# Kernel tuning notes

Measured on AMD Instinct MI355X. Metric: run time of the kernel, lower is better.

## Reference

```python
import jax, jax.numpy as jnp
import numpy as np


def setup_inputs() -> dict:
    key = jax.random.key(0)
    ks = jax.random.split(key, 5)
    B, T, I, H, O = 64, 1024, 128, 256, 128
    stdv = 1.0 / np.sqrt(H)
    return {
        "x": jax.random.normal(ks[0], (B, T, I), dtype=jnp.float32),
        "W": jax.random.uniform(ks[1], (I, 4 * H), dtype=jnp.float32, minval=-stdv, maxval=stdv),
        "U": jax.random.uniform(ks[2], (H, 4 * H), dtype=jnp.float32, minval=-stdv, maxval=stdv),
        "bias": jax.random.uniform(ks[3], (4 * H,), dtype=jnp.float32, minval=-stdv, maxval=stdv),
        "dense_w": jax.random.uniform(ks[4], (O, H), dtype=jnp.float32, minval=-stdv, maxval=stdv),
        "dense_b": jnp.zeros((O,), dtype=jnp.float32),
    }


def reference(x, W, U, bias, dense_w, dense_b):
    B, T, I = x.shape
    H = U.shape[0]
    # Precompute input contribution for all timesteps in one big GEMM.
    xW = jnp.einsum("bti,ig->btg", x, W) + bias  # (B, T, 4H)

    def step(carry, xw_t):
        h, c = carry
        gates = xw_t + h @ U  # (B, 4H)
        i_t = jax.nn.sigmoid(gates[:, :H])
        f_t = jax.nn.sigmoid(gates[:, H:2 * H])
        g_t = jnp.tanh(gates[:, 2 * H:3 * H])
        o_t = jax.nn.sigmoid(gates[:, 3 * H:])
        c = f_t * c + i_t * g_t
        h = o_t * jnp.tanh(c)
        return (h, c), h

    h0 = jnp.zeros((B, H), dtype=x.dtype)
    c0 = jnp.zeros((B, H), dtype=x.dtype)
    (h_T, _), _ = jax.lax.scan(step, (h0, c0), jnp.swapaxes(xW, 0, 1))
    # Original takes hidden_seq[:, -1, :] == final h_t, then Linear, then unsqueeze(2).
    out = h_T @ dense_w.T + dense_b  # (B, O)
    return out[:, :, None]  # (B, O, 1)
```

## Files before the change

### kernel.cpp

```cpp
#include <hip/hip_runtime.h>
#include <math.h>

#define TT 1024
#define BB 64
#define II 128
#define HH 256
#define OO 128
#define GPB 16
#define NCOL 64
#define Z_STRIDE 392
#define PART_BG_STRIDE 68
#define PART_RC_STRIDE 273

#define WS_HBUF_B 16384
#define WS_CLEAR_B (WS_HBUF_B + 2 * BB * HH * 8)

typedef unsigned long long u64;
typedef unsigned int u32;

__device__ __forceinline__ float rcp(float v) { return __builtin_amdgcn_rcpf(v); }
__device__ __forceinline__ float sigm(float v) { return rcp(1.f + __expf(-v)); }
__device__ __forceinline__ float ftanh(float v) {
    return __builtin_fmaf(-2.f, rcp(__expf(2.f * v) + 1.f), 1.f);
}

extern "C" __global__ void __launch_bounds__(256, 1) lstm_scan(
    const float* __restrict__ x, const float* __restrict__ W,
    const float* __restrict__ U, const float* __restrict__ bias,
    float* __restrict__ wsf)
{
    __shared__ float z[4 * Z_STRIDE];
    __shared__ float part[16 * PART_RC_STRIDE];
    __shared__ int   misc[8];

    int* abortp = (int*)wsf;
    u64* hbuf   = (u64*)((char*)wsf + WS_HBUF_B);

    const int tid  = threadIdx.x;
    const int gid  = blockIdx.x & 15;
    const int p    = blockIdx.x >> 4;
    const int cg   = tid & 15;
    const int rc   = tid >> 4;
    const int lane = tid & 63;
    const int w    = tid >> 6;
    const int myb  = 4 * gid + w;
    const int j    = lane & 15;

    float wr[6][4][4];
    {
        const int c0 = cg * 4;
        const int gcol = (c0 >> 4) * HH + p * 16 + (c0 & 15);
#pragma unroll
        for (int rr = 0; rr < 6; ++rr) {
#pragma unroll
            for (int i = 0; i < 4; ++i) {
                const int r = rr * 64 + rc * 4 + i;
                const float4 wv = (rr < 2)
                    ? *(const float4*)(W + (size_t)r * 1024 + gcol)
                    : *(const float4*)(U + (size_t)(r - II) * 1024 + gcol);
                wr[rr][i][0] = wv.x; wr[rr][i][1] = wv.y;
                wr[rr][i][2] = wv.z; wr[rr][i][3] = wv.w;
            }
        }
    }
    const float bia_reg = bias[(lane >> 4) * HH + p * 16 + j];
    float creg = 0.f;

    for (int idx = tid; idx < 4 * Z_STRIDE; idx += 256) z[idx] = 0.f;
    if (tid < 8) misc[tid] = 0;

    if (tid < 128) {
        const int b2 = tid >> 5, l2 = tid & 31;
        const float4 xv = *(const float4*)(
            x + ((size_t)(4 * gid + b2) * TT + 0) * II + 4 * l2);
        *(float4*)(z + b2 * Z_STRIDE + 4 * l2) = xv;
    }
    __syncthreads();

    for (int t = 1; t <= TT; ++t) {
        float acc[4][4];
#pragma unroll
        for (int a = 0; a < 4; ++a)
#pragma unroll
            for (int b = 0; b < 4; ++b) acc[a][b] = 0.f;

#pragma unroll
        for (int rr = 0; rr < 2; ++rr) {
#pragma unroll
            for (int bg = 0; bg < 4; ++bg) {
                const float4 zv = *(const float4*)(z + bg * Z_STRIDE + rr * 64 + rc * 4);
#pragma unroll
                for (int c = 0; c < 4; ++c)
                    acc[bg][c] += zv.x * wr[rr][0][c] + zv.y * wr[rr][1][c]
                                + zv.z * wr[rr][2][c] + zv.w * wr[rr][3][c];
            }
        }

        if (t > 1) {
            const u32 want = (u32)(t - 1);
            const u64* hsrc = hbuf + ((size_t)((t - 1) & 1) * BB + myb) * HH;
            u64 n0, n1, n2, n3;
            int it = 0, ab = 0;
            for (;;) {
                n0 = __hip_atomic_load(hsrc + lane,       __ATOMIC_RELAXED, __HIP_MEMORY_SCOPE_AGENT);
                n1 = __hip_atomic_load(hsrc + lane + 64,  __ATOMIC_RELAXED, __HIP_MEMORY_SCOPE_AGENT);
                n2 = __hip_atomic_load(hsrc + lane + 128, __ATOMIC_RELAXED, __HIP_MEMORY_SCOPE_AGENT);
                n3 = __hip_atomic_load(hsrc + lane + 192, __ATOMIC_RELAXED, __HIP_MEMORY_SCOPE_AGENT);
                const bool ok = ((u32)(n0 >> 32) == want) && ((u32)(n1 >> 32) == want)
                             && ((u32)(n2 >> 32) == want) && ((u32)(n3 >> 32) == want);
                if (__ballot(ok) == ~0ULL) break;
                if ((++it & 63) == 0) {
                    int abv = __hip_atomic_load(abortp, __ATOMIC_RELAXED,
                                                __HIP_MEMORY_SCOPE_AGENT);
                    if (abv) { ab = 1; break; }
                    if (it > (1 << 19)) {
                        if (lane == 0)
                            __hip_atomic_store(abortp, 1, __ATOMIC_RELAXED,
                                               __HIP_MEMORY_SCOPE_AGENT);
                        ab = 1; break;
                    }
                }
            }
            if (ab && lane == 0) misc[w] = 1;
            float* zdst = z + w * Z_STRIDE + II + lane;
            zdst[0]   = __uint_as_float((u32)n0);
            zdst[64]  = __uint_as_float((u32)n1);
            zdst[128] = __uint_as_float((u32)n2);
            zdst[192] = __uint_as_float((u32)n3);
        }
        __syncthreads();
        if (misc[0] | misc[1] | misc[2] | misc[3]) break;

#pragma unroll
        for (int rr = 2; rr < 6; ++rr) {
#pragma unroll
            for (int bg = 0; bg < 4; ++bg) {
                const float4 zv = *(const float4*)(z + bg * Z_STRIDE + rr * 64 + rc * 4);
#pragma unroll
                for (int c = 0; c < 4; ++c)
                    acc[bg][c] += zv.x * wr[rr][0][c] + zv.y * wr[rr][1][c]
                                + zv.z * wr[rr][2][c] + zv.w * wr[rr][3][c];
            }
        }

#pragma unroll
        for (int bg = 0; bg < 4; ++bg)
#pragma unroll
            for (int c = 0; c < 4; ++c)
                part[rc * PART_RC_STRIDE + bg * PART_BG_STRIDE + cg * 4 + c] = acc[bg][c];
        __syncthreads();

        float s = bia_reg;
#pragma unroll
        for (int r2 = 0; r2 < 16; ++r2)
            s += part[r2 * PART_RC_STRIDE + w * PART_BG_STRIDE + lane];

        const float sf = __shfl(s, j + 16);
        const float sg = __shfl(s, j + 32);
        const float so = __shfl(s, j + 48);
        if (lane < 16) {
            const float iv = sigm(s);
            const float fv = sigm(sf);
            const float gv = ftanh(sg);
            const float ov = sigm(so);
            creg = fv * creg + iv * gv;
            const float hv = ov * ftanh(creg);
            const u64 pk = ((u64)(u32)t << 32) | (u64)__float_as_uint(hv);
            __hip_atomic_store(
                hbuf + ((size_t)(t & 1) * BB + myb) * HH + p * 16 + j,
                pk, __ATOMIC_RELAXED, __HIP_MEMORY_SCOPE_AGENT);
        } else if (lane < 48 && t < TT) {
            const int l2 = lane - 16;
            const float4 xv = *(const float4*)(
                x + ((size_t)myb * TT + t) * II + 4 * l2);
            *(float4*)(z + w * Z_STRIDE + 4 * l2) = xv;
        }
        __syncthreads();
    }
}

extern "C" __global__ void __launch_bounds__(256) lstm_out(
    const float* __restrict__ wsf, const float* __restrict__ dw,
    const float* __restrict__ db, float* __restrict__ out)
{
    __shared__ float hs[256];
    __shared__ float red[256];
    const int b = blockIdx.x;
    const int tid = threadIdx.x;
    const u64* h0 = (const u64*)((const char*)wsf + WS_HBUF_B);
    hs[tid] = __uint_as_float((u32)h0[(size_t)b * HH + tid]);
    __syncthreads();
    const int o = tid & 127, half = tid >> 7;
    const float* wrow = dw + o * HH + half * 128;
    const float* hrow = hs + half * 128;
    float s = 0.f;
#pragma unroll
    for (int k = 0; k < 128; k += 4) {
        const float4 wv = *(const float4*)(wrow + k);
        s += hrow[k] * wv.x + hrow[k + 1] * wv.y + hrow[k + 2] * wv.z + hrow[k + 3] * wv.w;
    }
    red[tid] = s;
    __syncthreads();
    if (tid < 128)
        out[(size_t)b * OO + tid] = red[tid] + red[128 + tid] + db[tid];
}

extern "C" void kernel_launch(void* const* d_in, const int* in_sizes, int n_in,
                              void* d_out, int out_size, void* d_ws, size_t ws_size,
                              hipStream_t stream)
{
    const float* x    = (const float*)d_in[0];
    const float* W    = (const float*)d_in[1];
    const float* U    = (const float*)d_in[2];
    const float* bias = (const float*)d_in[3];
    const float* dw   = (const float*)d_in[4];
    const float* db   = (const float*)d_in[5];
    float* out = (float*)d_out;
    float* ws  = (float*)d_ws;

    hipMemsetAsync(d_ws, 0, WS_CLEAR_B, stream);
    hipLaunchKernelGGL(lstm_scan, dim3(256), dim3(256), 0, stream,
                       x, W, U, bias, ws);
    hipLaunchKernelGGL(lstm_out, dim3(64), dim3(256), 0, stream, ws, dw, db, out);
}
```

Baseline: 2.113 ms.

## Precompute x@W+bias with a separate GEMM kernel before the recurrent scan

Splits the input projection out of the persistent LSTM scan into a tiled GEMM kernel that writes x@W+bias to a 256MB workspace. The scan then only multiplies h by U each step and reads one precomputed gate value per thread, which shortens the per-step critical path and frees registers. The spin-wait also double-buffers its polling loads. The cost is an extra pass that writes and reads a large buffer through HBM. The old fused kernel is kept as a fallback when the workspace is too small.

```diff
diff --git a/kernel.cpp b/kernel.cpp
--- a/kernel.cpp
+++ b/kernel.cpp
@@ -9,11 +9,14 @@
 #define GPB 16
 #define NCOL 64
 #define Z_STRIDE 392
+#define ZS2 264
 #define PART_BG_STRIDE 68
 #define PART_RC_STRIDE 273
 
 #define WS_HBUF_B 16384
 #define WS_CLEAR_B (WS_HBUF_B + 2 * BB * HH * 8)
+#define WS_XW_B   524288
+#define WS_NEED   (524288ull + 268435456ull)
 
 typedef unsigned long long u64;
 typedef unsigned int u32;
@@ -23,13 +26,64 @@
 __device__ __forceinline__ float ftanh(float v) {
     return __builtin_fmaf(-2.f, rcp(__expf(2.f * v) + 1.f), 1.f);
 }
+#define HLOAD(p) __hip_atomic_load((p), __ATOMIC_RELAXED, __HIP_MEMORY_SCOPE_AGENT)
+
+extern "C" __global__ void __launch_bounds__(256) xw_gemm(
+    const float* __restrict__ x, const float* __restrict__ W,
+    const float* __restrict__ bias, float* __restrict__ xw)
+{
+    __shared__ float xs[64][65];
+    __shared__ float wt[64][68];
+    const int tid = threadIdx.x;
+    const int tx = tid & 15, ty = tid >> 4;
+    const int bm = blockIdx.x, bn = blockIdx.y;
+
+    float acc[4][4];
+#pragma unroll
+    for (int i = 0; i < 4; ++i)
+#pragma unroll
+        for (int jj = 0; jj < 4; ++jj) acc[i][jj] = 0.f;
+
+    for (int k0 = 0; k0 < 128; k0 += 64) {
+#pragma unroll
+        for (int l = 0; l < 4; ++l) {
+            const int e = tid + l * 256;
+            const int row = e >> 4, c4 = (e & 15) * 4;
+            *(float4*)&xs[row][c4] =
+                *(const float4*)(x + (size_t)(bm * 64 + row) * 128 + k0 + c4);
+            *(float4*)&wt[row][c4] =
+                *(const float4*)(W + (size_t)(k0 + row) * 1024 + bn * 64 + c4);
+        }
+        __syncthreads();
+#pragma unroll 16
+        for (int kk = 0; kk < 64; ++kk) {
+            const float4 bv = *(const float4*)&wt[kk][tx * 4];
+#pragma unroll
+            for (int i = 0; i < 4; ++i) {
+                const float av = xs[ty * 4 + i][kk];
+                acc[i][0] += av * bv.x; acc[i][1] += av * bv.y;
+                acc[i][2] += av * bv.z; acc[i][3] += av * bv.w;
+            }
+        }
+        __syncthreads();
+    }
+#pragma unroll
+    for (int i = 0; i < 4; ++i) {
+        const int row = bm * 64 + ty * 4 + i, col = bn * 64 + tx * 4;
+        float4 o;
+        o.x = acc[i][0] + bias[col];
+        o.y = acc[i][1] + bias[col + 1];
+        o.z = acc[i][2] + bias[col + 2];
+        o.w = acc[i][3] + bias[col + 3];
+        *(float4*)(xw + (size_t)row * 1024 + col) = o;
+    }
+}
 
 extern "C" __global__ void __launch_bounds__(256, 1) lstm_scan(
-    const float* __restrict__ x, const float* __restrict__ W,
-    const float* __restrict__ U, const float* __restrict__ bias,
+    const float* __restrict__ xw, const float* __restrict__ U,
     float* __restrict__ wsf)
 {
-    __shared__ float z[4 * Z_STRIDE];
+    __shared__ float z[4 * ZS2];
     __shared__ float part[16 * PART_RC_STRIDE];
     __shared__ int   misc[8];
 
@@ -46,72 +100,50 @@
     const int myb  = 4 * gid + w;
     const int j    = lane & 15;
 
-    float wr[6][4][4];
+    float wh[4][4][4];
     {
         const int c0 = cg * 4;
         const int gcol = (c0 >> 4) * HH + p * 16 + (c0 & 15);
 #pragma unroll
-        for (int rr = 0; rr < 6; ++rr) {
+        for (int rrh = 0; rrh < 4; ++rrh)
 #pragma unroll
             for (int i = 0; i < 4; ++i) {
-                const int r = rr * 64 + rc * 4 + i;
-                const float4 wv = (rr < 2)
-                    ? *(const float4*)(W + (size_t)r * 1024 + gcol)
-                    : *(const float4*)(U + (size_t)(r - II) * 1024 + gcol);
-                wr[rr][i][0] = wv.x; wr[rr][i][1] = wv.y;
-                wr[rr][i][2] = wv.z; wr[rr][i][3] = wv.w;
-            }
-        }
-    }
-    const float bia_reg = bias[(lane >> 4) * HH + p * 16 + j];
+                const int r = rrh * 64 + rc * 4 + i;
+                const float4 wv = *(const float4*)(U + (size_t)r * 1024 + gcol);
+                wh[rrh][i][0] = wv.x; wh[rrh][i][1] = wv.y;
+                wh[rrh][i][2] = wv.z; wh[rrh][i][3] = wv.w;
+            }
+    }
+    const int redcol = (lane >> 4) * HH + p * 16 + j;
     float creg = 0.f;
 
-    for (int idx = tid; idx < 4 * Z_STRIDE; idx += 256) z[idx] = 0.f;
+    for (int idx = tid; idx < 4 * ZS2; idx += 256) z[idx] = 0.f;
     if (tid < 8) misc[tid] = 0;
-
-    if (tid < 128) {
-        const int b2 = tid >> 5, l2 = tid & 31;
-        const float4 xv = *(const float4*)(
-            x + ((size_t)(4 * gid + b2) * TT + 0) * II + 4 * l2);
-        *(float4*)(z + b2 * Z_STRIDE + 4 * l2) = xv;
-    }
     __syncthreads();
 
+    float xwreg = xw[((size_t)myb * TT + 0) * 1024 + redcol];
+
     for (int t = 1; t <= TT; ++t) {
-        float acc[4][4];
-#pragma unroll
-        for (int a = 0; a < 4; ++a)
-#pragma unroll
-            for (int b = 0; b < 4; ++b) acc[a][b] = 0.f;
-
-#pragma unroll
-        for (int rr = 0; rr < 2; ++rr) {
-#pragma unroll
-            for (int bg = 0; bg < 4; ++bg) {
-                const float4 zv = *(const float4*)(z + bg * Z_STRIDE + rr * 64 + rc * 4);
-#pragma unroll
-                for (int c = 0; c < 4; ++c)
-                    acc[bg][c] += zv.x * wr[rr][0][c] + zv.y * wr[rr][1][c]
-                                + zv.z * wr[rr][2][c] + zv.w * wr[rr][3][c];
-            }
-        }
-
         if (t > 1) {
             const u32 want = (u32)(t - 1);
             const u64* hsrc = hbuf + ((size_t)((t - 1) & 1) * BB + myb) * HH;
             u64 n0, n1, n2, n3;
+            u64 a0 = HLOAD(hsrc + lane),       a1 = HLOAD(hsrc + lane + 64),
+                a2 = HLOAD(hsrc + lane + 128), a3 = HLOAD(hsrc + lane + 192);
             int it = 0, ab = 0;
             for (;;) {
-                n0 = __hip_atomic_load(hsrc + lane,       __ATOMIC_RELAXED, __HIP_MEMORY_SCOPE_AGENT);
-                n1 = __hip_atomic_load(hsrc + lane + 64,  __ATOMIC_RELAXED, __HIP_MEMORY_SCOPE_AGENT);
-                n2 = __hip_atomic_load(hsrc + lane + 128, __ATOMIC_RELAXED, __HIP_MEMORY_SCOPE_AGENT);
-                n3 = __hip_atomic_load(hsrc + lane + 192, __ATOMIC_RELAXED, __HIP_MEMORY_SCOPE_AGENT);
-                const bool ok = ((u32)(n0 >> 32) == want) && ((u32)(n1 >> 32) == want)
-                             && ((u32)(n2 >> 32) == want) && ((u32)(n3 >> 32) == want);
-                if (__ballot(ok) == ~0ULL) break;
+                u64 b0 = HLOAD(hsrc + lane),       b1 = HLOAD(hsrc + lane + 64),
+                    b2 = HLOAD(hsrc + lane + 128), b3 = HLOAD(hsrc + lane + 192);
+                bool ok = ((u32)(a0 >> 32) == want) && ((u32)(a1 >> 32) == want)
+                       && ((u32)(a2 >> 32) == want) && ((u32)(a3 >> 32) == want);
+                if (__ballot(ok) == ~0ULL) { n0 = a0; n1 = a1; n2 = a2; n3 = a3; break; }
+                a0 = HLOAD(hsrc + lane);       a1 = HLOAD(hsrc + lane + 64);
+                a2 = HLOAD(hsrc + lane + 128); a3 = HLOAD(hsrc + lane + 192);
+                ok = ((u32)(b0 >> 32) == want) && ((u32)(b1 >> 32) == want)
+                  && ((u32)(b2 >> 32) == want) && ((u32)(b3 >> 32) == want);
+                if (__ballot(ok) == ~0ULL) { n0 = b0; n1 = b1; n2 = b2; n3 = b3; break; }
                 if ((++it & 63) == 0) {
-                    int abv = __hip_atomic_load(abortp, __ATOMIC_RELAXED,
-                                                __HIP_MEMORY_SCOPE_AGENT);
+                    int abv = HLOAD(abortp);
                     if (abv) { ab = 1; break; }
                     if (it > (1 << 19)) {
                         if (lane == 0)
@@ -121,6 +153,154 @@
                     }
                 }
             }
+            if (ab) { if (lane == 0) misc[w] = 1; n0 = n1 = n2 = n3 = 0; }
+            float* zdst = z + w * ZS2 + lane;
+            zdst[0]   = __uint_as_float((u32)n0);
+            zdst[64]  = __uint_as_float((u32)n1);
+            zdst[128] = __uint_as_float((u32)n2);
+            zdst[192] = __uint_as_float((u32)n3);
+        }
+        __syncthreads();
+        if (misc[0] | misc[1] | misc[2] | misc[3]) break;
+
+        float acc[4][4];
+#pragma unroll
+        for (int a = 0; a < 4; ++a)
+#pragma unroll
+            for (int b = 0; b < 4; ++b) acc[a][b] = 0.f;
+#pragma unroll
+        for (int rrh = 0; rrh < 4; ++rrh) {
+#pragma unroll
+            for (int bg = 0; bg < 4; ++bg) {
+                const float4 zv = *(const float4*)(z + bg * ZS2 + rrh * 64 + rc * 4);
+#pragma unroll
+                for (int c = 0; c < 4; ++c)
+                    acc[bg][c] += zv.x * wh[rrh][0][c] + zv.y * wh[rrh][1][c]
+                                + zv.z * wh[rrh][2][c] + zv.w * wh[rrh][3][c];
+            }
+        }
+#pragma unroll
+        for (int bg = 0; bg < 4; ++bg)
+#pragma unroll
+            for (int c = 0; c < 4; ++c)
+                part[rc * PART_RC_STRIDE + bg * PART_BG_STRIDE + cg * 4 + c] = acc[bg][c];
+        __syncthreads();
+
+        float s = xwreg;
+#pragma unroll
+        for (int r2 = 0; r2 < 16; ++r2)
+            s += part[r2 * PART_RC_STRIDE + w * PART_BG_STRIDE + lane];
+
+        const float sf = __shfl(s, j + 16);
+        const float sg = __shfl(s, j + 32);
+        const float so = __shfl(s, j + 48);
+        if (lane < 16) {
+            const float iv = sigm(s);
+            const float fv = sigm(sf);
+            const float gv = ftanh(sg);
+            const float ov = sigm(so);
+            creg = fv * creg + iv * gv;
+            const float hv = ov * ftanh(creg);
+            const u64 pk = ((u64)(u32)t << 32) | (u64)__float_as_uint(hv);
+            __hip_atomic_store(
+                hbuf + ((size_t)(t & 1) * BB + myb) * HH + p * 16 + j,
+                pk, __ATOMIC_RELAXED, __HIP_MEMORY_SCOPE_AGENT);
+        }
+        if (t < TT)
+            xwreg = xw[((size_t)myb * TT + t) * 1024 + redcol];
+    }
+}
+
+extern "C" __global__ void __launch_bounds__(256, 1) lstm_scan_fb(
+    const float* __restrict__ x, const float* __restrict__ W,
+    const float* __restrict__ U, const float* __restrict__ bias,
+    float* __restrict__ wsf)
+{
+    __shared__ float z[4 * Z_STRIDE];
+    __shared__ float part[16 * PART_RC_STRIDE];
+    __shared__ int   misc[8];
+
+    int* abortp = (int*)wsf;
+    u64* hbuf   = (u64*)((char*)wsf + WS_HBUF_B);
+
+    const int tid  = threadIdx.x;
+    const int gid  = blockIdx.x & 15;
+    const int p    = blockIdx.x >> 4;
+    const int cg   = tid & 15;
+    const int rc   = tid >> 4;
+    const int lane = tid & 63;
+    const int w    = tid >> 6;
+    const int myb  = 4 * gid + w;
+    const int j    = lane & 15;
+
+    float wr[6][4][4];
+    {
+        const int c0 = cg * 4;
+        const int gcol = (c0 >> 4) * HH + p * 16 + (c0 & 15);
+#pragma unroll
+        for (int rr = 0; rr < 6; ++rr)
+#pragma unroll
+            for (int i = 0; i < 4; ++i) {
+                const int r = rr * 64 + rc * 4 + i;
+                const float4 wv = (rr < 2)
+                    ? *(const float4*)(W + (size_t)r * 1024 + gcol)
+                    : *(const float4*)(U + (size_t)(r - II) * 1024 + gcol);
+                wr[rr][i][0] = wv.x; wr[rr][i][1] = wv.y;
+                wr[rr][i][2] = wv.z; wr[rr][i][3] = wv.w;
+            }
+    }
+    const float bia_reg = bias[(lane >> 4) * HH + p * 16 + j];
+    float creg = 0.f;
+
+    for (int idx = tid; idx < 4 * Z_STRIDE; idx += 256) z[idx] = 0.f;
+    if (tid < 8) misc[tid] = 0;
+    if (tid < 128) {
+        const int b2 = tid >> 5, l2 = tid & 31;
+        const float4 xv = *(const float4*)(
+            x + ((size_t)(4 * gid + b2) * TT + 0) * II + 4 * l2);
+        *(float4*)(z + b2 * Z_STRIDE + 4 * l2) = xv;
+    }
+    __syncthreads();
+
+    for (int t = 1; t <= TT; ++t) {
+        float acc[4][4];
+#pragma unroll
+        for (int a = 0; a < 4; ++a)
+#pragma unroll
+            for (int b = 0; b < 4; ++b) acc[a][b] = 0.f;
+#pragma unroll
+        for (int rr = 0; rr < 2; ++rr)
+#pragma unroll
+            for (int bg = 0; bg < 4; ++bg) {
+                const float4 zv = *(const float4*)(z + bg * Z_STRIDE + rr * 64 + rc * 4);
+#pragma unroll
+                for (int c = 0; c < 4; ++c)
+                    acc[bg][c] += zv.x * wr[rr][0][c] + zv.y * wr[rr][1][c]
+                                + zv.z * wr[rr][2][c] + zv.w * wr[rr][3][c];
+            }
+
+        if (t > 1) {
+            const u32 want = (u32)(t - 1);
+            const u64* hsrc = hbuf + ((size_t)((t - 1) & 1) * BB + myb) * HH;
+            u64 n0, n1, n2, n3;
+            int it = 0, ab = 0;
+            for (;;) {
+                n0 = HLOAD(hsrc + lane);       n1 = HLOAD(hsrc + lane + 64);
+                n2 = HLOAD(hsrc + lane + 128); n3 = HLOAD(hsrc + lane + 192);
+                const bool ok = ((u32)(n0 >> 32) == want) && ((u32)(n1 >> 32) == want)
+                             && ((u32)(n2 >> 32) == want) && ((u32)(n3 >> 32) == want);
+                if (__ballot(ok) == ~0ULL) break;
+                if ((++it & 63) == 0) {
+                    int abv = HLOAD(abortp);
+                    if (abv) { ab = 1; break; }
+                    if (it > (1 << 19)) {
+                        if (lane == 0)
+                            __hip_atomic_store(abortp, 1, __ATOMIC_RELAXED,
+                                               __HIP_MEMORY_SCOPE_AGENT);
+                        ab = 1; break;
+                    }
+                }
+            }
             if (ab && lane == 0) misc[w] = 1;
             float* zdst = z + w * Z_STRIDE + II + lane;
             zdst[0]   = __uint_as_float((u32)n0);
@@ -132,7 +312,7 @@
         if (misc[0] | misc[1] | misc[2] | misc[3]) break;
 
 #pragma unroll
-        for (int rr = 2; rr < 6; ++rr) {
+        for (int rr = 2; rr < 6; ++rr)
 #pragma unroll
             for (int bg = 0; bg < 4; ++bg) {
                 const float4 zv = *(const float4*)(z + bg * Z_STRIDE + rr * 64 + rc * 4);
@@ -141,8 +321,6 @@
                     acc[bg][c] += zv.x * wr[rr][0][c] + zv.y * wr[rr][1][c]
                                 + zv.z * wr[rr][2][c] + zv.w * wr[rr][3][c];
             }
-        }
-
 #pragma unroll
         for (int bg = 0; bg < 4; ++bg)
 #pragma unroll
@@ -219,7 +397,15 @@
     float* ws  = (float*)d_ws;
 
     hipMemsetAsync(d_ws, 0, WS_CLEAR_B, stream);
-    hipLaunchKernelGGL(lstm_scan, dim3(256), dim3(256), 0, stream,
-                       x, W, U, bias, ws);
+    if (ws_size >= WS_NEED) {
+        float* xw = (float*)((char*)d_ws + WS_XW_B);
+        hipLaunchKernelGGL(xw_gemm, dim3(1024, 16), dim3(256), 0, stream,
+                           x, W, bias, xw);
+        hipLaunchKernelGGL(lstm_scan, dim3(256), dim3(256), 0, stream,
+                           xw, U, ws);
+    } else {
+        hipLaunchKernelGGL(lstm_scan_fb, dim3(256), dim3(256), 0, stream,
+                           x, W, U, bias, ws);
+    }
     hipLaunchKernelGGL(lstm_out, dim3(64), dim3(256), 0, stream, ws, dw, db, out);
 }
```

Result: no change. 2.121 ms (+0.4%).

## Double-buffer x tile, prefetch x early, pipeline h polling, drop trailing barrier

Applied to the files above, without the earlier changes.

The x slice for the next timestep now goes into a separate double-buffered shared array. It is loaded into registers at the start of the step and stored after the recurrent matmul, which takes the global x load off the critical path. With x in its own buffers, the per-step trailing __syncthreads can be removed. The spin-wait on the h buffer now keeps two sets of loads in flight, so each check overlaps with the next poll. The cost is extra shared memory and more registers, and correctness now depends on subtle barrier ordering.

```diff
diff --git a/kernel.cpp b/kernel.cpp
--- a/kernel.cpp
+++ b/kernel.cpp
@@ -7,8 +7,8 @@
 #define HH 256
 #define OO 128
 #define GPB 16
-#define NCOL 64
-#define Z_STRIDE 392
+#define ZSH 264
+#define XBS 132
 #define PART_BG_STRIDE 68
 #define PART_RC_STRIDE 273
 
@@ -23,13 +23,15 @@
 __device__ __forceinline__ float ftanh(float v) {
     return __builtin_fmaf(-2.f, rcp(__expf(2.f * v) + 1.f), 1.f);
 }
+#define HLOAD(p) __hip_atomic_load((p), __ATOMIC_RELAXED, __HIP_MEMORY_SCOPE_AGENT)
 
 extern "C" __global__ void __launch_bounds__(256, 1) lstm_scan(
     const float* __restrict__ x, const float* __restrict__ W,
     const float* __restrict__ U, const float* __restrict__ bias,
     float* __restrict__ wsf)
 {
-    __shared__ float z[4 * Z_STRIDE];
+    __shared__ float z[4 * ZSH];
+    __shared__ float xb[2][4 * XBS];
     __shared__ float part[16 * PART_RC_STRIDE];
     __shared__ int   misc[8];
 
@@ -45,13 +47,15 @@
     const int w    = tid >> 6;
     const int myb  = 4 * gid + w;
     const int j    = lane & 15;
+    const int b2   = tid >> 5;
+    const int l2   = tid & 31;
 
     float wr[6][4][4];
     {
         const int c0 = cg * 4;
         const int gcol = (c0 >> 4) * HH + p * 16 + (c0 & 15);
 #pragma unroll
-        for (int rr = 0; rr < 6; ++rr) {
+        for (int rr = 0; rr < 6; ++rr)
 #pragma unroll
             for (int i = 0; i < 4; ++i) {
                 const int r = rr * 64 + rc * 4 + i;
@@ -61,57 +65,64 @@
                 wr[rr][i][0] = wv.x; wr[rr][i][1] = wv.y;
                 wr[rr][i][2] = wv.z; wr[rr][i][3] = wv.w;
             }
-        }
     }
     const float bia_reg = bias[(lane >> 4) * HH + p * 16 + j];
     float creg = 0.f;
 
-    for (int idx = tid; idx < 4 * Z_STRIDE; idx += 256) z[idx] = 0.f;
+    for (int idx = tid; idx < 4 * ZSH; idx += 256) z[idx] = 0.f;
     if (tid < 8) misc[tid] = 0;
-
     if (tid < 128) {
-        const int b2 = tid >> 5, l2 = tid & 31;
         const float4 xv = *(const float4*)(
             x + ((size_t)(4 * gid + b2) * TT + 0) * II + 4 * l2);
-        *(float4*)(z + b2 * Z_STRIDE + 4 * l2) = xv;
+        *(float4*)(&xb[1][b2 * XBS + 4 * l2]) = xv;
     }
     __syncthreads();
 
     for (int t = 1; t <= TT; ++t) {
+        float4 xnext;
+        if (t < TT && tid < 128)
+            xnext = *(const float4*)(
+                x + ((size_t)(4 * gid + b2) * TT + t) * II + 4 * l2);
+
         float acc[4][4];
 #pragma unroll
         for (int a = 0; a < 4; ++a)
 #pragma unroll
             for (int b = 0; b < 4; ++b) acc[a][b] = 0.f;
-
-#pragma unroll
-        for (int rr = 0; rr < 2; ++rr) {
-#pragma unroll
-            for (int bg = 0; bg < 4; ++bg) {
-                const float4 zv = *(const float4*)(z + bg * Z_STRIDE + rr * 64 + rc * 4);
-#pragma unroll
-                for (int c = 0; c < 4; ++c)
-                    acc[bg][c] += zv.x * wr[rr][0][c] + zv.y * wr[rr][1][c]
-                                + zv.z * wr[rr][2][c] + zv.w * wr[rr][3][c];
-            }
+        {
+            const float* xcur = xb[t & 1];
+#pragma unroll
+            for (int rr = 0; rr < 2; ++rr)
+#pragma unroll
+                for (int bg = 0; bg < 4; ++bg) {
+                    const float4 zv = *(const float4*)(xcur + bg * XBS + rr * 64 + rc * 4);
+#pragma unroll
+                    for (int c = 0; c < 4; ++c)
+                        acc[bg][c] += zv.x * wr[rr][0][c] + zv.y * wr[rr][1][c]
+                                    + zv.z * wr[rr][2][c] + zv.w * wr[rr][3][c];
+                }
         }
 
         if (t > 1) {
             const u32 want = (u32)(t - 1);
             const u64* hsrc = hbuf + ((size_t)((t - 1) & 1) * BB + myb) * HH;
             u64 n0, n1, n2, n3;
+            u64 a0 = HLOAD(hsrc + lane),       a1 = HLOAD(hsrc + lane + 64),
+                a2 = HLOAD(hsrc + lane + 128), a3 = HLOAD(hsrc + lane + 192);
             int it = 0, ab = 0;
             for (;;) {
-                n0 = __hip_atomic_load(hsrc + lane,       __ATOMIC_RELAXED, __HIP_MEMORY_SCOPE_AGENT);
-                n1 = __hip_atomic_load(hsrc + lane + 64,  __ATOMIC_RELAXED, __HIP_MEMORY_SCOPE_AGENT);
-                n2 = __hip_atomic_load(hsrc + lane + 128, __ATOMIC_RELAXED, __HIP_MEMORY_SCOPE_AGENT);
-                n3 = __hip_atomic_load(hsrc + lane + 192, __ATOMIC_RELAXED, __HIP_MEMORY_SCOPE_AGENT);
-                const bool ok = ((u32)(n0 >> 32) == want) && ((u32)(n1 >> 32) == want)
-                             && ((u32)(n2 >> 32) == want) && ((u32)(n3 >> 32) == want);
-                if (__ballot(ok) == ~0ULL) break;
+                u64 c0 = HLOAD(hsrc + lane),       c1 = HLOAD(hsrc + lane + 64),
+                    c2 = HLOAD(hsrc + lane + 128), c3 = HLOAD(hsrc + lane + 192);
+                bool ok = ((u32)(a0 >> 32) == want) && ((u32)(a1 >> 32) == want)
+                       && ((u32)(a2 >> 32) == want) && ((u32)(a3 >> 32) == want);
+                if (__ballot(ok) == ~0ULL) { n0 = a0; n1 = a1; n2 = a2; n3 = a3; break; }
+                a0 = HLOAD(hsrc + lane);       a1 = HLOAD(hsrc + lane + 64);
+                a2 = HLOAD(hsrc + lane + 128); a3 = HLOAD(hsrc + lane + 192);
+                ok = ((u32)(c0 >> 32) == want) && ((u32)(c1 >> 32) == want)
+                  && ((u32)(c2 >> 32) == want) && ((u32)(c3 >> 32) == want);
+                if (__ballot(ok) == ~0ULL) { n0 = c0; n1 = c1; n2 = c2; n3 = c3; break; }
                 if ((++it & 63) == 0) {
-                    int abv = __hip_atomic_load(abortp, __ATOMIC_RELAXED,
-                                                __HIP_MEMORY_SCOPE_AGENT);
+                    int abv = HLOAD(abortp);
                     if (abv) { ab = 1; break; }
                     if (it > (1 << 19)) {
                         if (lane == 0)
@@ -121,8 +132,8 @@
                     }
                 }
             }
-            if (ab && lane == 0) misc[w] = 1;
-            float* zdst = z + w * Z_STRIDE + II + lane;
+            if (ab) { if (lane == 0) misc[w] = 1; n0 = n1 = n2 = n3 = 0; }
+            float* zdst = z + w * ZSH + lane;
             zdst[0]   = __uint_as_float((u32)n0);
             zdst[64]  = __uint_as_float((u32)n1);
             zdst[128] = __uint_as_float((u32)n2);
@@ -132,16 +143,18 @@
         if (misc[0] | misc[1] | misc[2] | misc[3]) break;
 
 #pragma unroll
-        for (int rr = 2; rr < 6; ++rr) {
+        for (int rrh = 0; rrh < 4; ++rrh)
 #pragma unroll
             for (int bg = 0; bg < 4; ++bg) {
-                const float4 zv = *(const float4*)(z + bg * Z_STRIDE + rr * 64 + rc * 4);
+                const float4 zv = *(const float4*)(z + bg * ZSH + rrh * 64 + rc * 4);
 #pragma unroll
                 for (int c = 0; c < 4; ++c)
-                    acc[bg][c] += zv.x * wr[rr][0][c] + zv.y * wr[rr][1][c]
-                                + zv.z * wr[rr][2][c] + zv.w * wr[rr][3][c];
+                    acc[bg][c] += zv.x * wr[rrh + 2][0][c] + zv.y * wr[rrh + 2][1][c]
+                                + zv.z * wr[rrh + 2][2][c] + zv.w * wr[rrh + 2][3][c];
             }
-        }
+
+        if (t < TT && tid < 128)
+            *(float4*)(&xb[(t + 1) & 1][b2 * XBS + 4 * l2]) = xnext;
 
 #pragma unroll
         for (int bg = 0; bg < 4; ++bg)
@@ -169,13 +182,7 @@
             __hip_atomic_store(
                 hbuf + ((size_t)(t & 1) * BB + myb) * HH + p * 16 + j,
                 pk, __ATOMIC_RELAXED, __HIP_MEMORY_SCOPE_AGENT);
-        } else if (lane < 48 && t < TT) {
-            const int l2 = lane - 16;
-            const float4 xv = *(const float4*)(
-                x + ((size_t)myb * TT + t) * II + 4 * l2);
-            *(float4*)(z + w * Z_STRIDE + 4 * l2) = xv;
         }
-        __syncthreads();
     }
 }
 
```

Result: slower. 2.293 ms (+8.5%).

## Split LSTM scan into 512 blocks with two batches each, two blocks per CU

Applied to the files above, without the earlier changes.

The persistent recurrent scan is repartitioned so that each block owns 2 batch rows instead of 4, and the grid doubles from 256 to 512 blocks. Launch bounds now allow 2 blocks per CU, so two blocks share a CU and can hide each other's latency. Per block, the per-step FMA work, the shared-memory z/part buffers and the number of polling waves are all halved. Waves 2–3 now only prefetch the next x rows while waves 0–1 reduce the gates and publish h. This relies on all 512 spinning blocks being co-resident, and doubles the number of blocks polling the shared h buffer each step.

```diff
diff --git a/kernel.cpp b/kernel.cpp
--- a/kernel.cpp
+++ b/kernel.cpp
@@ -6,11 +6,9 @@
 #define II 128
 #define HH 256
 #define OO 128
-#define GPB 16
-#define NCOL 64
 #define Z_STRIDE 392
 #define PART_BG_STRIDE 68
-#define PART_RC_STRIDE 273
+#define PART_RC_STRIDE 137
 
 #define WS_HBUF_B 16384
 #define WS_CLEAR_B (WS_HBUF_B + 2 * BB * HH * 8)
@@ -23,13 +21,14 @@
 __device__ __forceinline__ float ftanh(float v) {
     return __builtin_fmaf(-2.f, rcp(__expf(2.f * v) + 1.f), 1.f);
 }
-
-extern "C" __global__ void __launch_bounds__(256, 1) lstm_scan(
+#define HLOAD(p) __hip_atomic_load((p), __ATOMIC_RELAXED, __HIP_MEMORY_SCOPE_AGENT)
+
+extern "C" __global__ void __launch_bounds__(256, 2) lstm_scan(
     const float* __restrict__ x, const float* __restrict__ W,
     const float* __restrict__ U, const float* __restrict__ bias,
     float* __restrict__ wsf)
 {
-    __shared__ float z[4 * Z_STRIDE];
+    __shared__ float z[2 * Z_STRIDE];
     __shared__ float part[16 * PART_RC_STRIDE];
     __shared__ int   misc[8];
 
@@ -37,13 +36,13 @@
     u64* hbuf   = (u64*)((char*)wsf + WS_HBUF_B);
 
     const int tid  = threadIdx.x;
-    const int gid  = blockIdx.x & 15;
-    const int p    = blockIdx.x >> 4;
+    const int g    = blockIdx.x & 31;
+    const int p    = blockIdx.x >> 5;
     const int cg   = tid & 15;
     const int rc   = tid >> 4;
     const int lane = tid & 63;
     const int w    = tid >> 6;
-    const int myb  = 4 * gid + w;
+    const int myb  = 2 * g + (w & 1);
     const int j    = lane & 15;
 
     float wr[6][4][4];
@@ -51,7 +50,7 @@
         const int c0 = cg * 4;
         const int gcol = (c0 >> 4) * HH + p * 16 + (c0 & 15);
 #pragma unroll
-        for (int rr = 0; rr < 6; ++rr) {
+        for (int rr = 0; rr < 6; ++rr)
 #pragma unroll
             for (int i = 0; i < 4; ++i) {
                 const int r = rr * 64 + rc * 4 + i;
@@ -61,57 +60,51 @@
                 wr[rr][i][0] = wv.x; wr[rr][i][1] = wv.y;
                 wr[rr][i][2] = wv.z; wr[rr][i][3] = wv.w;
             }
-        }
     }
     const float bia_reg = bias[(lane >> 4) * HH + p * 16 + j];
     float creg = 0.f;
 
-    for (int idx = tid; idx < 4 * Z_STRIDE; idx += 256) z[idx] = 0.f;
+    for (int idx = tid; idx < 2 * Z_STRIDE; idx += 256) z[idx] = 0.f;
     if (tid < 8) misc[tid] = 0;
-
-    if (tid < 128) {
+    if (tid < 64) {
         const int b2 = tid >> 5, l2 = tid & 31;
         const float4 xv = *(const float4*)(
-            x + ((size_t)(4 * gid + b2) * TT + 0) * II + 4 * l2);
+            x + ((size_t)(2 * g + b2) * TT + 0) * II + 4 * l2);
         *(float4*)(z + b2 * Z_STRIDE + 4 * l2) = xv;
     }
     __syncthreads();
 
     for (int t = 1; t <= TT; ++t) {
-        float acc[4][4];
-#pragma unroll
-        for (int a = 0; a < 4; ++a)
+        float acc[2][4];
+#pragma unroll
+        for (int a = 0; a < 2; ++a)
 #pragma unroll
             for (int b = 0; b < 4; ++b) acc[a][b] = 0.f;
 
 #pragma unroll
-        for (int rr = 0; rr < 2; ++rr) {
-#pragma unroll
-            for (int bg = 0; bg < 4; ++bg) {
+        for (int rr = 0; rr < 2; ++rr)
+#pragma unroll
+            for (int bg = 0; bg < 2; ++bg) {
                 const float4 zv = *(const float4*)(z + bg * Z_STRIDE + rr * 64 + rc * 4);
 #pragma unroll
                 for (int c = 0; c < 4; ++c)
                     acc[bg][c] += zv.x * wr[rr][0][c] + zv.y * wr[rr][1][c]
                                 + zv.z * wr[rr][2][c] + zv.w * wr[rr][3][c];
             }
-        }
-
-        if (t > 1) {
+
+        if (t > 1 && w < 2) {
             const u32 want = (u32)(t - 1);
             const u64* hsrc = hbuf + ((size_t)((t - 1) & 1) * BB + myb) * HH;
             u64 n0, n1, n2, n3;
             int it = 0, ab = 0;
             for (;;) {
-                n0 = __hip_atomic_load(hsrc + lane,       __ATOMIC_RELAXED, __HIP_MEMORY_SCOPE_AGENT);
-                n1 = __hip_atomic_load(hsrc + lane + 64,  __ATOMIC_RELAXED, __HIP_MEMORY_SCOPE_AGENT);
-                n2 = __hip_atomic_load(hsrc + lane + 128, __ATOMIC_RELAXED, __HIP_MEMORY_SCOPE_AGENT);
-                n3 = __hip_atomic_load(hsrc + lane + 192, __ATOMIC_RELAXED, __HIP_MEMORY_SCOPE_AGENT);
+                n0 = HLOAD(hsrc + lane);       n1 = HLOAD(hsrc + lane + 64);
+                n2 = HLOAD(hsrc + lane + 128); n3 = HLOAD(hsrc + lane + 192);
                 const bool ok = ((u32)(n0 >> 32) == want) && ((u32)(n1 >> 32) == want)
                              && ((u32)(n2 >> 32) == want) && ((u32)(n3 >> 32) == want);
                 if (__ballot(ok) == ~0ULL) break;
                 if ((++it & 63) == 0) {
-                    int abv = __hip_atomic_load(abortp, __ATOMIC_RELAXED,
-                                                __HIP_MEMORY_SCOPE_AGENT);
+                    int abv = HLOAD(abortp);
                     if (abv) { ab = 1; break; }
                     if (it > (1 << 19)) {
                         if (lane == 0)
@@ -122,58 +115,59 @@
                 }
             }
             if (ab && lane == 0) misc[w] = 1;
-            float* zdst = z + w * Z_STRIDE + II + lane;
+            float* zdst = z + (w & 1) * Z_STRIDE + II + lane;
             zdst[0]   = __uint_as_float((u32)n0);
             zdst[64]  = __uint_as_float((u32)n1);
             zdst[128] = __uint_as_float((u32)n2);
             zdst[192] = __uint_as_float((u32)n3);
         }
         __syncthreads();
-        if (misc[0] | misc[1] | misc[2] | misc[3]) break;
-
-#pragma unroll
-        for (int rr = 2; rr < 6; ++rr) {
-#pragma unroll
-            for (int bg = 0; bg < 4; ++bg) {
+        if (misc[0] | misc[1]) break;
+
+#pragma unroll
+        for (int rr = 2; rr < 6; ++rr)
+#pragma unroll
+            for (int bg = 0; bg < 2; ++bg) {
                 const float4 zv = *(const float4*)(z + bg * Z_STRIDE + rr * 64 + rc * 4);
 #pragma unroll
                 for (int c = 0; c < 4; ++c)
                     acc[bg][c] += zv.x * wr[rr][0][c] + zv.y * wr[rr][1][c]
                                 + zv.z * wr[rr][2][c] + zv.w * wr[rr][3][c];
             }
-        }
-
-#pragma unroll
-        for (int bg = 0; bg < 4; ++bg)
+
+#pragma unroll
+        for (int bg = 0; bg < 2; ++bg)
 #pragma unroll
             for (int c = 0; c < 4; ++c)
                 part[rc * PART_RC_STRIDE + bg * PART_BG_STRIDE + cg * 4 + c] = acc[bg][c];
         __syncthreads();
 
-        float s = bia_reg;
-#pragma unroll
-        for (int r2 = 0; r2 < 16; ++r2)
-            s += part[r2 * PART_RC_STRIDE + w * PART_BG_STRIDE + lane];
-
-        const float sf = __shfl(s, j + 16);
-        const float sg = __shfl(s, j + 32);
-        const float so = __shfl(s, j + 48);
-        if (lane < 16) {
-            const float iv = sigm(s);
-            const float fv = sigm(sf);
-            const float gv = ftanh(sg);
-            const float ov = sigm(so);
-            creg = fv * creg + iv * gv;
-            const float hv = ov * ftanh(creg);
-            const u64 pk = ((u64)(u32)t << 32) | (u64)__float_as_uint(hv);
-            __hip_atomic_store(
-                hbuf + ((size_t)(t & 1) * BB + myb) * HH + p * 16 + j,
-                pk, __ATOMIC_RELAXED, __HIP_MEMORY_SCOPE_AGENT);
-        } else if (lane < 48 && t < TT) {
-            const int l2 = lane - 16;
+        if (w < 2) {
+            float s = bia_reg;
+#pragma unroll
+            for (int r2 = 0; r2 < 16; ++r2)
+                s += part[r2 * PART_RC_STRIDE + w * PART_BG_STRIDE + lane];
+
+            const float sf = __shfl(s, j + 16);
+            const float sg = __shfl(s, j + 32);
+            const float so = __shfl(s, j + 48);
+            if (lane < 16) {
+                const float iv = sigm(s);
+                const float fv = sigm(sf);
+                const float gv = ftanh(sg);
+                const float ov = sigm(so);
+                creg = fv * creg + iv * gv;
+                const float hv = ov * ftanh(creg);
+                const u64 pk = ((u64)(u32)t << 32) | (u64)__float_as_uint(hv);
+                __hip_atomic_store(
+                    hbuf + ((size_t)(t & 1) * BB + myb) * HH + p * 16 + j,
+                    pk, __ATOMIC_RELAXED, __HIP_MEMORY_SCOPE_AGENT);
+            }
+        } else if (t < TT && lane < 32) {
+            const int b2 = w - 2;
             const float4 xv = *(const float4*)(
-                x + ((size_t)myb * TT + t) * II + 4 * l2);
-            *(float4*)(z + w * Z_STRIDE + 4 * l2) = xv;
+                x + ((size_t)(2 * g + b2) * TT + t) * II + 4 * lane);
+            *(float4*)(z + b2 * Z_STRIDE + 4 * lane) = xv;
         }
         __syncthreads();
     }
@@ -219,7 +213,7 @@
     float* ws  = (float*)d_ws;
 
     hipMemsetAsync(d_ws, 0, WS_CLEAR_B, stream);
-    hipLaunchKernelGGL(lstm_scan, dim3(256), dim3(256), 0, stream,
+    hipLaunchKernelGGL(lstm_scan, dim3(512), dim3(256), 0, stream,
                        x, W, U, bias, ws);
     hipLaunchKernelGGL(lstm_out, dim3(64), dim3(256), 0, stream, ws, dw, db, out);
 }
```

Result: slower. 2.208 ms (+4.5%).
